# Kernel optimization log

Measured on AMD Instinct MI355X. Metric: run time of the kernel, lower is better.

The kernel has to match this reference:

```python
import jax, jax.numpy as jnp
import numpy as np
from jax import lax

D_MODEL = 1024
D_INNER = 2048   # expand=2.0
D_CONV = 4
D_STATE = 16     # delta=16
DT_RANK = 64     # ceil(d_model/16)
B, L = 4, 2048


def setup_inputs() -> dict:
    key = jax.random.key(0)
    ks = jax.random.split(key, 8)
    x = jax.random.normal(ks[0], (B, L, D_MODEL), jnp.float32)
    W_in = jax.random.normal(ks[1], (2 * D_INNER, D_MODEL), jnp.float32) * 0.02
    conv_w = jax.random.normal(ks[2], (D_INNER, D_CONV), jnp.float32) * 0.2
    conv_b = jnp.zeros((D_INNER,), jnp.float32)
    W_x = jax.random.normal(ks[3], (DT_RANK + 2 * D_STATE, D_INNER), jnp.float32) * 0.02
    W_dt = jax.random.normal(ks[4], (D_INNER, DT_RANK), jnp.float32) * 0.1
    # bias so softplus(b_dt) ~ dt in [1e-3, 1e-1] as in mamba_ssm init
    b_dt = jax.random.normal(ks[5], (D_INNER,), jnp.float32) * 0.3 - 4.0
    # mamba S4D-real init: A = -(1..d_state)
    A_log = jnp.log(jnp.tile(jnp.arange(1, D_STATE + 1, dtype=jnp.float32), (D_INNER, 1)))
    D_skip = jnp.ones((D_INNER,), jnp.float32)
    W_out = jax.random.normal(ks[6], (D_MODEL, D_INNER), jnp.float32) * 0.02
    return {"x": x, "W_in": W_in, "conv_w": conv_w, "conv_b": conv_b,
            "W_x": W_x, "W_dt": W_dt, "b_dt": b_dt, "A_log": A_log,
            "D_skip": D_skip, "W_out": W_out}


def reference(x, W_in, conv_w, conv_b, W_x, W_dt, b_dt, A_log, D_skip, W_out):
    Bsz, Lseq, _ = x.shape
    # input projection -> (B, L, 2*d_inner); split into ssm branch xi and gate z
    xz = jnp.einsum('bld,ed->ble', x, W_in)
    xi, z = jnp.split(xz, 2, axis=-1)
    # causal depthwise conv over sequence (pad left by d_conv-1), then SiLU
    xc = lax.conv_general_dilated(
        xi.transpose(0, 2, 1),               # (B, d_inner, L)
        conv_w[:, None, :],                  # (d_inner, 1, d_conv)
        window_strides=(1,),
        padding=[(D_CONV - 1, 0)],
        dimension_numbers=('NCH', 'OIH', 'NCH'),
        feature_group_count=D_INNER)
    xc = jax.nn.silu(xc + conv_b[None, :, None]).transpose(0, 2, 1)  # (B, L, d_inner)
    # data-dependent SSM params
    xdbl = jnp.einsum('bld,ed->ble', xc, W_x)          # (B, L, dt_rank + 2*d_state)
    dt_lo = xdbl[..., :DT_RANK]
    Bm = xdbl[..., DT_RANK:DT_RANK + D_STATE]          # (B, L, d_state)
    Cm = xdbl[..., DT_RANK + D_STATE:]                 # (B, L, d_state)
    dt = jax.nn.softplus(jnp.einsum('blr,dr->bld', dt_lo, W_dt) + b_dt)  # (B, L, d_inner)
    A = -jnp.exp(A_log)                                # (d_inner, d_state)

    def step(h, inp):
        dt_t, x_t, B_t, C_t = inp                      # (B,Di), (B,Di), (B,S), (B,S)
        dA = jnp.exp(dt_t[..., None] * A)              # (B, Di, S)
        h = dA * h + (dt_t * x_t)[..., None] * B_t[:, None, :]
        y = jnp.einsum('bds,bs->bd', h, C_t)
        return h, y

    h0 = jnp.zeros((Bsz, D_INNER, D_STATE), x.dtype)
    inputs = (dt.transpose(1, 0, 2), xc.transpose(1, 0, 2),
              Bm.transpose(1, 0, 2), Cm.transpose(1, 0, 2))
    _, ys = lax.scan(step, h0, inputs)                 # ys: (L, B, d_inner)
    y = ys.transpose(1, 0, 2) + xc * D_skip            # skip connection
    y = y * jax.nn.silu(z)                             # gating
    return jnp.einsum('bld,ed->ble', y, W_out)         # (B, L, d_model)
```

## Files before the change

### kernel.cpp

```cpp
#include <hip/hip_runtime.h>
#include <hip/hip_bf16.h>

#define DM    1024
#define DI    2048
#define DCONV 4
#define DSTATE 16
#define DRANK 64
#define BB    4
#define LSEQ  2048
#define MM    (BB*LSEQ)
#define CHUNK 64

typedef _Float16 f16x8 __attribute__((ext_vector_type(8)));
typedef _Float16 f16x4 __attribute__((ext_vector_type(4)));
typedef float    f32x4 __attribute__((ext_vector_type(4)));

#define SWIZMASK(row) (((row) & 3) ^ (((row) >> 2) & 1))
#define SWIZ(row, g)  ((((row) * 4) + ((g) ^ SWIZMASK(row))) * 8)

#define GLOAD_LDS16(gp, sp) __builtin_amdgcn_global_load_lds( \
    (const __attribute__((address_space(1))) void*)(gp),      \
    (__attribute__((address_space(3))) void*)(sp), 16, 0, 0)

__global__ __launch_bounds__(256) void split_kernel(
    const float* __restrict__ in, _Float16* __restrict__ hi,
    _Float16* __restrict__ lo, int n4)
{
    const int i = blockIdx.x * 256 + threadIdx.x;
    if (i >= n4) return;
    const float4 v = ((const float4*)in)[i];
    _Float16 h[4], l[4];
    h[0] = (_Float16)v.x; l[0] = (_Float16)(v.x - (float)h[0]);
    h[1] = (_Float16)v.y; l[1] = (_Float16)(v.y - (float)h[1]);
    h[2] = (_Float16)v.z; l[2] = (_Float16)(v.z - (float)h[2]);
    h[3] = (_Float16)v.w; l[3] = (_Float16)(v.w - (float)h[3]);
    *(uint2*)&hi[(size_t)i * 4] = *(uint2*)h;
    *(uint2*)&lo[(size_t)i * 4] = *(uint2*)l;
}

__global__ __launch_bounds__(256) void gemm_nt_split(
    float* __restrict__ C,
    const _Float16* __restrict__ Ah, const _Float16* __restrict__ Al,
    const _Float16* __restrict__ Bh, const _Float16* __restrict__ Bl,
    int M, int N, int K)
{
    __shared__ __align__(16) _Float16 sAh[128 * 32];
    __shared__ __align__(16) _Float16 sAl[128 * 32];
    __shared__ __align__(16) _Float16 sBh[128 * 32];
    __shared__ __align__(16) _Float16 sBl[128 * 32];

    const int t = threadIdx.x;
    const int m0 = blockIdx.y * 128, n0 = blockIdx.x * 128;
    const int l = t & 63, w = t >> 6;
    const int wr = w >> 1, wc = w & 1;
    const int fr = l & 15, fg = l >> 4;

    f32x4 acc[4][4];
    const f32x4 zz = {0.f, 0.f, 0.f, 0.f};
#pragma unroll
    for (int i = 0; i < 4; ++i)
#pragma unroll
        for (int j = 0; j < 4; ++j) acc[i][j] = zz;

    const int ch0 = w * 2, ch1 = w * 2 + 1;
    const int g4 = l & 3;
    const int rA0 = ch0 * 16 + (l >> 2), rA1 = ch1 * 16 + (l >> 2);
    const int c0 = (g4 ^ SWIZMASK(rA0)) * 8, c1 = (g4 ^ SWIZMASK(rA1)) * 8;
    const size_t gA0 = (size_t)(m0 + rA0) * K + c0;
    const size_t gA1 = (size_t)(m0 + rA1) * K + c1;
    const size_t gB0 = (size_t)(n0 + rA0) * K + c0;
    const size_t gB1 = (size_t)(n0 + rA1) * K + c1;
    const int lo0 = ch0 * 512, lo1 = ch1 * 512;

    const int nk = K / 32;
    for (int kt = 0; kt < nk; ++kt) {
        const size_t ko = (size_t)kt * 32;
        GLOAD_LDS16(&Ah[gA0 + ko], &sAh[lo0]);
        GLOAD_LDS16(&Ah[gA1 + ko], &sAh[lo1]);
        GLOAD_LDS16(&Al[gA0 + ko], &sAl[lo0]);
        GLOAD_LDS16(&Al[gA1 + ko], &sAl[lo1]);
        GLOAD_LDS16(&Bh[gB0 + ko], &sBh[lo0]);
        GLOAD_LDS16(&Bh[gB1 + ko], &sBh[lo1]);
        GLOAD_LDS16(&Bl[gB0 + ko], &sBl[lo0]);
        GLOAD_LDS16(&Bl[gB1 + ko], &sBl[lo1]);
        __syncthreads();

        f16x8 fbh[4], fbl[4];
#pragma unroll
        for (int nr = 0; nr < 4; ++nr) {
            const int row = wc * 64 + nr * 16 + fr;
            const int ad = SWIZ(row, fg);
            fbh[nr] = *(const f16x8*)&sBh[ad];
            fbl[nr] = *(const f16x8*)&sBl[ad];
        }
#pragma unroll
        for (int mr = 0; mr < 4; ++mr) {
            const int row = wr * 64 + mr * 16 + fr;
            const int ad = SWIZ(row, fg);
            const f16x8 fah = *(const f16x8*)&sAh[ad];
            const f16x8 fal = *(const f16x8*)&sAl[ad];
#pragma unroll
            for (int nr = 0; nr < 4; ++nr) {
                acc[mr][nr] = __builtin_amdgcn_mfma_f32_16x16x32_f16(
                    fah, fbh[nr], acc[mr][nr], 0, 0, 0);
                acc[mr][nr] = __builtin_amdgcn_mfma_f32_16x16x32_f16(
                    fah, fbl[nr], acc[mr][nr], 0, 0, 0);
                acc[mr][nr] = __builtin_amdgcn_mfma_f32_16x16x32_f16(
                    fal, fbh[nr], acc[mr][nr], 0, 0, 0);
            }
        }
        __syncthreads();
    }

#pragma unroll
    for (int mr = 0; mr < 4; ++mr)
#pragma unroll
        for (int nr = 0; nr < 4; ++nr) {
            const int col = n0 + wc * 64 + nr * 16 + fr;
#pragma unroll
            for (int q = 0; q < 4; ++q) {
                const int rowc = m0 + wr * 64 + mr * 16 + fg * 4 + q;
                C[(size_t)rowc * N + col] = acc[mr][nr][q];
            }
        }
}

__global__ __launch_bounds__(256) void dt_mfma_kernel(
    const float* __restrict__ xdbl, const float* __restrict__ Wdt,
    const float* __restrict__ bdt, float* __restrict__ dtout)
{
    __shared__ __align__(16) _Float16 sAh[128 * 32];
    __shared__ __align__(16) _Float16 sAl[128 * 32];
    __shared__ __align__(16) _Float16 sBh[128 * 32];
    __shared__ __align__(16) _Float16 sBl[128 * 32];

    const int t = threadIdx.x;
    const int m0 = blockIdx.y * 128, n0 = blockIdx.x * 128;
    const int l = t & 63, w = t >> 6;
    const int wr = w >> 1, wc = w & 1;
    const int fr = l & 15, fg = l >> 4;

    f32x4 acc[4][4];
    const f32x4 zz = {0.f, 0.f, 0.f, 0.f};
#pragma unroll
    for (int i = 0; i < 4; ++i)
#pragma unroll
        for (int j = 0; j < 4; ++j) acc[i][j] = zz;

#pragma unroll
    for (int kt = 0; kt < 2; ++kt) {
        __syncthreads();
#pragma unroll
        for (int ss = 0; ss < 2; ++ss) {
            const int s = t + ss * 256;
            const int row = s >> 2, c = s & 3;
            const int dst = SWIZ(row, c);
            {
                const float* p = &xdbl[(size_t)(m0 + row) * 96 + kt * 32 + c * 8];
                const float4 a0 = *(const float4*)p, a1 = *(const float4*)(p + 4);
                _Float16 h[8], lo8[8];
                const float vv[8] = {a0.x,a0.y,a0.z,a0.w,a1.x,a1.y,a1.z,a1.w};
#pragma unroll
                for (int q = 0; q < 8; ++q) {
                    h[q] = (_Float16)vv[q]; lo8[q] = (_Float16)(vv[q] - (float)h[q]);
                }
                *(uint4*)&sAh[dst] = *(uint4*)h;
                *(uint4*)&sAl[dst] = *(uint4*)lo8;
            }
            {
                const float* p = &Wdt[(size_t)(n0 + row) * 64 + kt * 32 + c * 8];
                const float4 b0 = *(const float4*)p, b1 = *(const float4*)(p + 4);
                _Float16 h[8], lo8[8];
                const float vv[8] = {b0.x,b0.y,b0.z,b0.w,b1.x,b1.y,b1.z,b1.w};
#pragma unroll
                for (int q = 0; q < 8; ++q) {
                    h[q] = (_Float16)vv[q]; lo8[q] = (_Float16)(vv[q] - (float)h[q]);
                }
                *(uint4*)&sBh[dst] = *(uint4*)h;
                *(uint4*)&sBl[dst] = *(uint4*)lo8;
            }
        }
        __syncthreads();

        f16x8 fbh[4], fbl[4];
#pragma unroll
        for (int nr = 0; nr < 4; ++nr) {
            const int row = wc * 64 + nr * 16 + fr;
            const int ad = SWIZ(row, fg);
            fbh[nr] = *(const f16x8*)&sBh[ad];
            fbl[nr] = *(const f16x8*)&sBl[ad];
        }
#pragma unroll
        for (int mr = 0; mr < 4; ++mr) {
            const int row = wr * 64 + mr * 16 + fr;
            const int ad = SWIZ(row, fg);
            const f16x8 fah = *(const f16x8*)&sAh[ad];
            const f16x8 fal = *(const f16x8*)&sAl[ad];
#pragma unroll
            for (int nr = 0; nr < 4; ++nr) {
                acc[mr][nr] = __builtin_amdgcn_mfma_f32_16x16x32_f16(
                    fah, fbh[nr], acc[mr][nr], 0, 0, 0);
                acc[mr][nr] = __builtin_amdgcn_mfma_f32_16x16x32_f16(
                    fah, fbl[nr], acc[mr][nr], 0, 0, 0);
                acc[mr][nr] = __builtin_amdgcn_mfma_f32_16x16x32_f16(
                    fal, fbh[nr], acc[mr][nr], 0, 0, 0);
            }
        }
    }

#pragma unroll
    for (int mr = 0; mr < 4; ++mr)
#pragma unroll
        for (int nr = 0; nr < 4; ++nr) {
            const int col = n0 + wc * 64 + nr * 16 + fr;
            const float bd = bdt[col];
#pragma unroll
            for (int q = 0; q < 4; ++q) {
                const int rowc = m0 + wr * 64 + mr * 16 + fg * 4 + q;
                const float v = acc[mr][nr][q] + bd;
                dtout[(size_t)rowc * DI + col] =
                    (v > 20.f) ? v : log1pf(__expf(v));
            }
        }
}

__global__ __launch_bounds__(256) void conv_silu_split_kernel(
    const float* __restrict__ xi, const float* __restrict__ cw,
    const float* __restrict__ cb, _Float16* __restrict__ xch,
    _Float16* __restrict__ xcl)
{
    const int idx = blockIdx.x * 256 + threadIdx.x;
    const int d4 = idx & (DI / 4 - 1);
    const int bl = idx / (DI / 4);
    const int l  = bl & (LSEQ - 1);
    const int d  = d4 * 4;

    float4 acc = *(const float4*)&cb[d];
    const float4 w0 = *(const float4*)&cw[(d + 0) * 4];
    const float4 w1 = *(const float4*)&cw[(d + 1) * 4];
    const float4 w2 = *(const float4*)&cw[(d + 2) * 4];
    const float4 w3 = *(const float4*)&cw[(d + 3) * 4];

#pragma unroll
    for (int k = 0; k < 4; ++k) {
        const int ll = l - 3 + k;
        if (ll < 0) continue;
        const float4 xv = *(const float4*)&xi[(size_t)(bl - 3 + k) * DI + d];
        const float wk0 = (k == 0) ? w0.x : (k == 1) ? w0.y : (k == 2) ? w0.z : w0.w;
        const float wk1 = (k == 0) ? w1.x : (k == 1) ? w1.y : (k == 2) ? w1.z : w1.w;
        const float wk2 = (k == 0) ? w2.x : (k == 1) ? w2.y : (k == 2) ? w2.z : w2.w;
        const float wk3 = (k == 0) ? w3.x : (k == 1) ? w3.y : (k == 2) ? w3.z : w3.w;
        acc.x = fmaf(xv.x, wk0, acc.x);
        acc.y = fmaf(xv.y, wk1, acc.y);
        acc.z = fmaf(xv.z, wk2, acc.z);
        acc.w = fmaf(xv.w, wk3, acc.w);
    }
    acc.x = acc.x / (1.f + __expf(-acc.x));
    acc.y = acc.y / (1.f + __expf(-acc.y));
    acc.z = acc.z / (1.f + __expf(-acc.z));
    acc.w = acc.w / (1.f + __expf(-acc.w));

    _Float16 h[4], lo4[4];
    h[0] = (_Float16)acc.x; lo4[0] = (_Float16)(acc.x - (float)h[0]);
    h[1] = (_Float16)acc.y; lo4[1] = (_Float16)(acc.y - (float)h[1]);
    h[2] = (_Float16)acc.z; lo4[2] = (_Float16)(acc.z - (float)h[2]);
    h[3] = (_Float16)acc.w; lo4[3] = (_Float16)(acc.w - (float)h[3]);
    *(uint2*)&xch[(size_t)bl * DI + d] = *(uint2*)h;
    *(uint2*)&xcl[(size_t)bl * DI + d] = *(uint2*)lo4;
}

__global__ __launch_bounds__(256) void xdbl_mfma_kernel(
    const _Float16* __restrict__ Xh, const _Float16* __restrict__ Xl,
    const _Float16* __restrict__ Wh, const _Float16* __restrict__ Wl,
    float* __restrict__ xdbl)
{
    __shared__ __align__(16) _Float16 sXh[64 * 32];
    __shared__ __align__(16) _Float16 sXl[64 * 32];
    __shared__ __align__(16) _Float16 sWh[96 * 32];
    __shared__ __align__(16) _Float16 sWl[96 * 32];

    const int t = threadIdx.x;
    const int m0 = blockIdx.x * 64;
    const int l = t & 63, w = t >> 6;
    const int fr = l & 15, fg = l >> 4;

    f32x4 acc[6];
    const f32x4 zz = {0.f, 0.f, 0.f, 0.f};
#pragma unroll
    for (int i = 0; i < 6; ++i) acc[i] = zz;

    const int ar = t >> 2, ac = t & 3;
    const int da = SWIZ(ar, ac);
    const size_t gX = (size_t)(m0 + ar) * DI + ac * 8;
    const int br0 = t >> 2, bc0 = t & 3;
    const int db0 = SWIZ(br0, bc0);
    const size_t gW0 = (size_t)br0 * DI + bc0 * 8;
    const bool has1 = t < 128;
    const int br1 = (t + 256) >> 2, bc1 = t & 3;
    const int db1 = SWIZ(br1, bc1);
    const size_t gW1 = (size_t)br1 * DI + bc1 * 8;

    uint4 vXh = *(const uint4*)&Xh[gX], vXl = *(const uint4*)&Xl[gX];
    uint4 vWh0 = *(const uint4*)&Wh[gW0], vWl0 = *(const uint4*)&Wl[gW0];
    uint4 vWh1, vWl1;
    if (has1) { vWh1 = *(const uint4*)&Wh[gW1]; vWl1 = *(const uint4*)&Wl[gW1]; }

    const int nk = DI / 32;
    for (int kt = 0; kt < nk; ++kt) {
        __syncthreads();
        *(uint4*)&sXh[da] = vXh;   *(uint4*)&sXl[da] = vXl;
        *(uint4*)&sWh[db0] = vWh0; *(uint4*)&sWl[db0] = vWl0;
        if (has1) { *(uint4*)&sWh[db1] = vWh1; *(uint4*)&sWl[db1] = vWl1; }
        __syncthreads();

        if (kt + 1 < nk) {
            const size_t o = (size_t)(kt + 1) * 32;
            vXh = *(const uint4*)&Xh[gX + o];   vXl = *(const uint4*)&Xl[gX + o];
            vWh0 = *(const uint4*)&Wh[gW0 + o]; vWl0 = *(const uint4*)&Wl[gW0 + o];
            if (has1) { vWh1 = *(const uint4*)&Wh[gW1 + o]; vWl1 = *(const uint4*)&Wl[gW1 + o]; }
        }

        const int aad = SWIZ(w * 16 + fr, fg);
        const f16x8 fah = *(const f16x8*)&sXh[aad];
        const f16x8 fal = *(const f16x8*)&sXl[aad];
#pragma unroll
        for (int nr = 0; nr < 6; ++nr) {
            const int bad = SWIZ(nr * 16 + fr, fg);
            const f16x8 fbh = *(const f16x8*)&sWh[bad];
            const f16x8 fbl = *(const f16x8*)&sWl[bad];
            acc[nr] = __builtin_amdgcn_mfma_f32_16x16x32_f16(fah, fbh, acc[nr], 0, 0, 0);
            acc[nr] = __builtin_amdgcn_mfma_f32_16x16x32_f16(fah, fbl, acc[nr], 0, 0, 0);
            acc[nr] = __builtin_amdgcn_mfma_f32_16x16x32_f16(fal, fbh, acc[nr], 0, 0, 0);
        }
    }

#pragma unroll
    for (int nr = 0; nr < 6; ++nr) {
        const int col = nr * 16 + fr;
#pragma unroll
        for (int q = 0; q < 4; ++q) {
            const int row = m0 + w * 16 + fg * 4 + q;
            xdbl[(size_t)row * 96 + col] = acc[nr][q];
        }
    }
}

__global__ __launch_bounds__(256) void scan_kernel(
    const float* __restrict__ dt,
    const _Float16* __restrict__ xch, const _Float16* __restrict__ xcl,
    const float* __restrict__ xdbl, const float* z,
    const float* __restrict__ A_log, const float* __restrict__ D_skip,
    float* y)
{
    __shared__ float s_dt[CHUNK][16];
    __shared__ float s_xc[CHUNK][20];
    __shared__ float s_z [CHUNK][20];
    __shared__ float s_B [CHUNK][16];
    __shared__ float s_C [CHUNK][16];
    __shared__ float s_p [16][16][17];
    __shared__ float s_D [16];

    const int t = threadIdx.x;
    const int g = t >> 4;
    const int s = t & 15;
    const int c = blockIdx.x * 16 + g;
    const int b = c >> 11;
    const int d = c & (DI - 1);
    const int d0 = (blockIdx.x * 16) & (DI - 1);

    const int lr = t >> 2;
    const int lc = t & 3;

    if (t < 16) s_D[t] = D_skip[d0 + t];

    const float Acoef = -__expf(A_log[d * DSTATE + s]);
    const size_t rbase = (size_t)b * LSEQ;

    float h = 0.f;
    float4 r_dt, r_z, r_B, r_C;
    f16x4 r_xh, r_xl;

    {
        const size_t row = rbase + lr;
        r_dt = *(const float4*)&dt[row * DI + d0 + lc * 4];
        r_xh = *(const f16x4*)&xch[row * DI + d0 + lc * 4];
        r_xl = *(const f16x4*)&xcl[row * DI + d0 + lc * 4];
        r_z  = *(const float4*)&z [row * DI + d0 + lc * 4];
        r_B  = *(const float4*)&xdbl[row * 96 + DRANK + lc * 4];
        r_C  = *(const float4*)&xdbl[row * 96 + DRANK + DSTATE + lc * 4];
    }

    for (int ch = 0; ch < LSEQ / CHUNK; ++ch) {
        __syncthreads();
        *(float4*)&s_dt[lr][lc * 4] = r_dt;
        {
            float4 xf;
            xf.x = (float)r_xh[0] + (float)r_xl[0];
            xf.y = (float)r_xh[1] + (float)r_xl[1];
            xf.z = (float)r_xh[2] + (float)r_xl[2];
            xf.w = (float)r_xh[3] + (float)r_xl[3];
            *(float4*)&s_xc[lr][lc * 4] = xf;
        }
        *(float4*)&s_z [lr][lc * 4] = r_z;
        *(float4*)&s_B [lr][lc * 4] = r_B;
        *(float4*)&s_C [lr][lc * 4] = r_C;
        __syncthreads();

        if (ch + 1 < LSEQ / CHUNK) {
            const size_t row = rbase + (size_t)(ch + 1) * CHUNK + lr;
            r_dt = *(const float4*)&dt[row * DI + d0 + lc * 4];
            r_xh = *(const f16x4*)&xch[row * DI + d0 + lc * 4];
            r_xl = *(const f16x4*)&xcl[row * DI + d0 + lc * 4];
            r_z  = *(const float4*)&z [row * DI + d0 + lc * 4];
            r_B  = *(const float4*)&xdbl[row * 96 + DRANK + lc * 4];
            r_C  = *(const float4*)&xdbl[row * 96 + DRANK + DSTATE + lc * 4];
        }

#pragma unroll
        for (int sub = 0; sub < CHUNK / 16; ++sub) {
            const int base = sub * 16;
            float dA[16], u[16], Cv[16];
#pragma unroll
            for (int j = 0; j < 16; ++j) {
                const float dtv = s_dt[base + j][g];
                const float xv  = s_xc[base + j][g];
                const float Bv  = s_B [base + j][s];
                Cv[j] = s_C[base + j][s];
                dA[j] = __expf(dtv * Acoef);
                u[j]  = dtv * xv * Bv;
            }
#pragma unroll
            for (int j = 0; j < 16; ++j) {
                h = fmaf(dA[j], h, u[j]);
                s_p[g][j][s] = h * Cv[j];
            }
            __syncthreads();
            float accp = 0.f;
#pragma unroll
            for (int k = 0; k < 16; ++k)
                accp += s_p[g][s][k];
            {
                const int row = base + s;
                const float xv = s_xc[row][g];
                const float zv = s_z [row][g];
                const float sig = 1.f / (1.f + __expf(-zv));
                s_z[row][g] = fmaf(xv, s_D[g], accp) * (zv * sig);
            }
            __syncthreads();
        }
        {
            const size_t row = rbase + (size_t)ch * CHUNK + lr;
            *(float4*)&y[row * DI + d0 + lc * 4] = *(const float4*)&s_z[lr][lc * 4];
        }
    }
}

extern "C" void kernel_launch(void* const* d_in, const int* in_sizes, int n_in,
                              void* d_out, int out_size, void* d_ws, size_t ws_size,
                              hipStream_t stream)
{
    const float* x      = (const float*)d_in[0];
    const float* W_in   = (const float*)d_in[1];
    const float* cw     = (const float*)d_in[2];
    const float* cb     = (const float*)d_in[3];
    const float* W_x    = (const float*)d_in[4];
    const float* W_dt   = (const float*)d_in[5];
    const float* b_dt   = (const float*)d_in[6];
    const float* A_log  = (const float*)d_in[7];
    const float* D_skip = (const float*)d_in[8];
    const float* W_out  = (const float*)d_in[9];
    float* out = (float*)d_out;

    const size_t MMDI = (size_t)MM * DI;
    float* xi  = (float*)d_ws;
    float* zb  = xi  + MMDI;
    float* xcb = zb  + MMDI;
    float* xdb = xcb + MMDI;

    _Float16* xh   = (_Float16*)xcb;
    _Float16* xl   = xh + (size_t)MM * DM;
    _Float16* Winh = xl + (size_t)MM * DM;
    _Float16* Winl = Winh + (size_t)2 * DI * DM;
    _Float16* xch  = (_Float16*)xcb;
    _Float16* xcl  = xch + MMDI;
    _Float16* Wxh  = (_Float16*)xi;
    _Float16* Wxl  = Wxh + (size_t)96 * DI;
    _Float16* yh   = (_Float16*)xcb;
    _Float16* yl   = yh + MMDI;
    _Float16* Woh  = (_Float16*)xi;
    _Float16* Wol  = Woh + (size_t)DM * DI;

    const dim3 blk(256);

    split_kernel<<<dim3((MM * DM / 4) / 256), blk, 0, stream>>>(x, xh, xl, MM * DM / 4);
    split_kernel<<<dim3((2 * DI * DM / 4) / 256), blk, 0, stream>>>(
        W_in, Winh, Winl, 2 * DI * DM / 4);

    gemm_nt_split<<<dim3(DI / 128, MM / 128), blk, 0, stream>>>(
        xi, xh, xl, Winh, Winl, MM, DI, DM);
    gemm_nt_split<<<dim3(DI / 128, MM / 128), blk, 0, stream>>>(
        zb, xh, xl, Winh + (size_t)DI * DM, Winl + (size_t)DI * DM, MM, DI, DM);

    conv_silu_split_kernel<<<dim3(MM * (DI / 4) / 256), blk, 0, stream>>>(
        xi, cw, cb, xch, xcl);

    split_kernel<<<dim3((96 * DI / 4) / 256), blk, 0, stream>>>(
        W_x, Wxh, Wxl, 96 * DI / 4);

    xdbl_mfma_kernel<<<dim3(MM / 64), blk, 0, stream>>>(xch, xcl, Wxh, Wxl, xdb);

    dt_mfma_kernel<<<dim3(DI / 128, MM / 128), blk, 0, stream>>>(
        xdb, W_dt, b_dt, xi);

    scan_kernel<<<dim3(BB * DI / 16), blk, 0, stream>>>(
        xi, xch, xcl, xdb, zb, A_log, D_skip, zb);

    split_kernel<<<dim3((MM * DI / 4) / 256), blk, 0, stream>>>(zb, yh, yl, MM * DI / 4);
    split_kernel<<<dim3((DM * DI / 4) / 256), blk, 0, stream>>>(
        W_out, Woh, Wol, DM * DI / 4);

    gemm_nt_split<<<dim3(DM / 128, MM / 128), blk, 0, stream>>>(
        out, yh, yl, Woh, Wol, MM, DM, DI);
}
```

Measured before the change: 788.9 us.

## Fuse fp16 hi/lo split of y into scan and pack scan inputs in LDS

```diff
diff --git a/kernel.cpp b/kernel.cpp
--- a/kernel.cpp
+++ b/kernel.cpp
@@ -347,16 +347,15 @@
 
 __global__ __launch_bounds__(256) void scan_kernel(
     const float* __restrict__ dt,
-    const _Float16* __restrict__ xch, const _Float16* __restrict__ xcl,
-    const float* __restrict__ xdbl, const float* z,
+    const _Float16* xch, const _Float16* xcl,
+    const float* __restrict__ xdbl, const float* __restrict__ z,
     const float* __restrict__ A_log, const float* __restrict__ D_skip,
-    float* y)
-{
-    __shared__ float s_dt[CHUNK][16];
+    _Float16* yh, _Float16* yl)
+{
+    __shared__ float s_du[CHUNK][16][2];
+    __shared__ float s_bc[CHUNK][16][2];
     __shared__ float s_xc[CHUNK][20];
     __shared__ float s_z [CHUNK][20];
-    __shared__ float s_B [CHUNK][16];
-    __shared__ float s_C [CHUNK][16];
     __shared__ float s_p [16][16][17];
     __shared__ float s_D [16];
 
@@ -392,18 +391,25 @@
 
     for (int ch = 0; ch < LSEQ / CHUNK; ++ch) {
         __syncthreads();
-        *(float4*)&s_dt[lr][lc * 4] = r_dt;
         {
-            float4 xf;
-            xf.x = (float)r_xh[0] + (float)r_xl[0];
-            xf.y = (float)r_xh[1] + (float)r_xl[1];
-            xf.z = (float)r_xh[2] + (float)r_xl[2];
-            xf.w = (float)r_xh[3] + (float)r_xl[3];
-            *(float4*)&s_xc[lr][lc * 4] = xf;
-        }
-        *(float4*)&s_z [lr][lc * 4] = r_z;
-        *(float4*)&s_B [lr][lc * 4] = r_B;
-        *(float4*)&s_C [lr][lc * 4] = r_C;
+            float xf[4];
+            xf[0] = (float)r_xh[0] + (float)r_xl[0];
+            xf[1] = (float)r_xh[1] + (float)r_xl[1];
+            xf[2] = (float)r_xh[2] + (float)r_xl[2];
+            xf[3] = (float)r_xh[3] + (float)r_xl[3];
+            const float dtv[4] = {r_dt.x, r_dt.y, r_dt.z, r_dt.w};
+            const float Bv[4]  = {r_B.x, r_B.y, r_B.z, r_B.w};
+            const float Cv[4]  = {r_C.x, r_C.y, r_C.z, r_C.w};
+#pragma unroll
+            for (int i = 0; i < 4; ++i) {
+                float2 du = {dtv[i], dtv[i] * xf[i]};
+                *(float2*)&s_du[lr][lc * 4 + i][0] = du;
+                float2 bc = {Bv[i], Cv[i]};
+                *(float2*)&s_bc[lr][lc * 4 + i][0] = bc;
+            }
+            *(float4*)&s_xc[lr][lc * 4] = *(float4*)xf;
+            *(float4*)&s_z [lr][lc * 4] = r_z;
+        }
         __syncthreads();
 
         if (ch + 1 < LSEQ / CHUNK) {
@@ -419,20 +425,13 @@
 #pragma unroll
         for (int sub = 0; sub < CHUNK / 16; ++sub) {
             const int base = sub * 16;
-            float dA[16], u[16], Cv[16];
 #pragma unroll
             for (int j = 0; j < 16; ++j) {
-                const float dtv = s_dt[base + j][g];
-                const float xv  = s_xc[base + j][g];
-                const float Bv  = s_B [base + j][s];
-                Cv[j] = s_C[base + j][s];
-                dA[j] = __expf(dtv * Acoef);
-                u[j]  = dtv * xv * Bv;
-            }
-#pragma unroll
-            for (int j = 0; j < 16; ++j) {
-                h = fmaf(dA[j], h, u[j]);
-                s_p[g][j][s] = h * Cv[j];
+                const float2 du = *(const float2*)&s_du[base + j][g][0];
+                const float2 bc = *(const float2*)&s_bc[base + j][s][0];
+                const float dA = __expf(du.x * Acoef);
+                h = fmaf(dA, h, du.y * bc.x);
+                s_p[g][j][s] = h * bc.y;
             }
             __syncthreads();
             float accp = 0.f;
@@ -450,7 +449,16 @@
         }
         {
             const size_t row = rbase + (size_t)ch * CHUNK + lr;
-            *(float4*)&y[row * DI + d0 + lc * 4] = *(const float4*)&s_z[lr][lc * 4];
+            const float4 yv = *(const float4*)&s_z[lr][lc * 4];
+            _Float16 hh[4], ll[4];
+            const float vv[4] = {yv.x, yv.y, yv.z, yv.w};
+#pragma unroll
+            for (int q = 0; q < 4; ++q) {
+                hh[q] = (_Float16)vv[q];
+                ll[q] = (_Float16)(vv[q] - (float)hh[q]);
+            }
+            *(uint2*)&yh[row * DI + d0 + lc * 4] = *(uint2*)hh;
+            *(uint2*)&yl[row * DI + d0 + lc * 4] = *(uint2*)ll;
         }
     }
 }
@@ -513,9 +521,8 @@
         xdb, W_dt, b_dt, xi);
 
     scan_kernel<<<dim3(BB * DI / 16), blk, 0, stream>>>(
-        xi, xch, xcl, xdb, zb, A_log, D_skip, zb);
-
-    split_kernel<<<dim3((MM * DI / 4) / 256), blk, 0, stream>>>(zb, yh, yl, MM * DI / 4);
+        xi, xch, xcl, xdb, zb, A_log, D_skip, yh, yl);
+
     split_kernel<<<dim3((DM * DI / 4) / 256), blk, 0, stream>>>(
         W_out, Woh, Wol, DM * DI / 4);
 
```

New measurement: 762.8 us. -3.3%, faster.
